# Performance work log

Measured on AMD Instinct MI355X. Metric: run time of the kernel, lower is better.

Reference implementation:

```python
import jax, jax.numpy as jnp
import numpy as np

EMBED_DIM = 1024
HEAD_DIM = 128

def setup_inputs() -> dict:
    key = jax.random.key(0)
    ks = jax.random.split(key, 7)
    B, S = 4, 2048
    x = jax.random.normal(ks[0], (B, S, EMBED_DIM), dtype=jnp.float32)
    # Linear params: weight [embed_dim, head_dim] (applied as x @ W + b), scaled init
    scale = 1.0 / np.sqrt(EMBED_DIM)
    Wq = jax.random.normal(ks[1], (EMBED_DIM, HEAD_DIM), dtype=jnp.float32) * scale
    Wk = jax.random.normal(ks[2], (EMBED_DIM, HEAD_DIM), dtype=jnp.float32) * scale
    Wv = jax.random.normal(ks[3], (EMBED_DIM, HEAD_DIM), dtype=jnp.float32) * scale
    bq = jax.random.normal(ks[4], (HEAD_DIM,), dtype=jnp.float32) * 0.01
    bk = jax.random.normal(ks[5], (HEAD_DIM,), dtype=jnp.float32) * 0.01
    bv = jax.random.normal(ks[6], (HEAD_DIM,), dtype=jnp.float32) * 0.01
    return {"x": x, "Wq": Wq, "bq": bq, "Wk": Wk, "bk": bk, "Wv": Wv, "bv": bv}

def reference(x, Wq, bq, Wk, bk, Wv, bv):
    # x: [B, S, E]
    S = x.shape[1]
    norm = jnp.asarray(HEAD_DIM ** 0.5, x.dtype)
    q = x @ Wq + bq  # [B, S, D]
    k = x @ Wk + bk
    v = x @ Wv + bv
    scores = jnp.einsum('bsd,btd->bst', q, k) / norm  # [B, S, S]
    causal = jnp.tril(jnp.ones((S, S), dtype=bool))
    scores = jnp.where(causal, scores, -jnp.inf)
    att = jax.nn.softmax(scores, axis=-1)
    return jnp.einsum('bst,btd->bsd', att, v)  # [B, S, D]
```

## Files before the change

### kernel.cpp

```cpp
#include <hip/hip_runtime.h>
#include <hip/hip_bf16.h>

typedef __attribute__((ext_vector_type(8))) short short8;
typedef __attribute__((ext_vector_type(4))) float f32x4;

static __device__ __forceinline__ unsigned short f2bf(float f){
  union { float f; unsigned int u; } v; v.f = f;
  unsigned int r = v.u + 0x7fffu + ((v.u >> 16) & 1u);
  return (unsigned short)(r >> 16);
}

static __device__ __forceinline__ void load_lds16(const unsigned short* g, unsigned short* l){
  __builtin_amdgcn_global_load_lds(
      (const __attribute__((address_space(1))) unsigned int*)(g),
      (__attribute__((address_space(3))) unsigned int*)(l), 16, 0, 0);
}

__global__ void k_prep(const float* __restrict__ Wq, const float* __restrict__ Wk,
                       const float* __restrict__ Wv,
                       const float* __restrict__ bq, const float* __restrict__ bk,
                       const float* __restrict__ bv,
                       unsigned short* __restrict__ Wt, float* __restrict__ bias){
  int gid = blockIdx.x * 256 + threadIdx.x;
  int p = gid >> 17;
  int rem = gid & 131071;
  int d = rem >> 10, e = rem & 1023;
  const float* W = (p==0) ? Wq : ((p==1) ? Wk : Wv);
  Wt[gid] = f2bf(W[e*128 + d]);
  if (gid < 384){
    int pp = gid >> 7, dd = gid & 127;
    bias[gid] = (pp==0) ? bq[dd] : ((pp==1) ? bk[dd] : bv[dd]);
  }
}

__global__ __launch_bounds__(256) void k_gemm_qkv(
    const float* __restrict__ x, const unsigned short* __restrict__ Wt,
    const float* __restrict__ bias,
    unsigned short* __restrict__ Qsw, unsigned short* __restrict__ Ksw,
    unsigned short* __restrict__ Vsw){
  __shared__ __align__(16) char smem[51200];
  float* Lf = (float*)smem;
  int tid = threadIdx.x;
  int bid = blockIdx.x;
  int xcd = bid & 7;
  int slot = bid >> 3;
  int mtl = slot / 3;
  int p   = slot - mtl*3;
  int mt  = xcd*16 + mtl;
  int m0 = mt * 64;
  int w = tid >> 6, lane = tid & 63, quad = lane >> 4, l16 = lane & 15;
  int wm = (w >> 1) * 32, wn = (w & 1) * 64;
  f32x4 acc[2][4];
  #pragma unroll
  for (int i=0;i<2;i++)
    #pragma unroll
    for (int j=0;j<4;j++) acc[i][j] = (f32x4){0.f,0.f,0.f,0.f};

  int arow = tid >> 2;
  int acg  = tid & 3;
  const float* Ax = x + (size_t)(m0 + arow)*1024 + acg*16;
  float4 av[4];

  const unsigned short* Wp = Wt + p * (128*1024);
  const unsigned short* Bg = Wp + (w*32 + (lane>>3))*1024 + (lane&7)*8;
  int boff = (w*32)*64;

  auto aload = [&](int k0){
    #pragma unroll
    for (int i=0;i<4;i++) av[i] = *(const float4*)(Ax + k0 + i*4);
  };
  auto astore = [&](int sel){
    unsigned short h[16];
    #pragma unroll
    for (int i=0;i<4;i++){
      h[i*4+0]=f2bf(av[i].x); h[i*4+1]=f2bf(av[i].y);
      h[i*4+2]=f2bf(av[i].z); h[i*4+3]=f2bf(av[i].w);
    }
    unsigned short* Ad = (unsigned short*)(smem + sel*25600) + arow*72 + acg*16;
    *(uint4*)(Ad)   = *(uint4*)(h);
    *(uint4*)(Ad+8) = *(uint4*)(h+8);
  };
  auto bstage = [&](int sel, int k0){
    unsigned short* Bl = (unsigned short*)(smem + sel*25600 + 9216) + boff;
    #pragma unroll
    for (int s8=0; s8<4; s8++) load_lds16(Bg + k0 + s8*8192, Bl + s8*512);
  };

  aload(0); bstage(0, 0); astore(0);
  __syncthreads();
  int cur = 0;
  for (int t=0; t<16; t++){
    if (t < 15){ aload((t+1)*64); bstage(cur^1, (t+1)*64); }
    const unsigned short* Ac = (const unsigned short*)(smem + cur*25600);
    const unsigned short* Bc = Ac + 4608;
    #pragma unroll
    for (int kk=0; kk<64; kk+=32){
      short8 af[2], bf[4];
      #pragma unroll
      for (int i=0;i<2;i++) af[i] = *(const short8*)(Ac + (wm + i*16 + l16)*72 + kk + quad*8);
      #pragma unroll
      for (int j=0;j<4;j++) bf[j] = *(const short8*)(Bc + (wn + j*16 + l16)*64 + kk + quad*8);
      #pragma unroll
      for (int i=0;i<2;i++)
        #pragma unroll
        for (int j=0;j<4;j++)
          acc[i][j] = __builtin_amdgcn_mfma_f32_16x16x32_bf16(af[i], bf[j], acc[i][j], 0,0,0);
    }
    if (t < 15) astore(cur^1);
    __syncthreads();
    cur ^= 1;
  }

  const float qscale = 0.08838834764831845f;
  if (p == 2){
    #pragma unroll
    for (int i=0;i<2;i++)
      #pragma unroll
      for (int j=0;j<4;j++){
        int grow0 = m0 + wm + i*16 + quad*4;
        int col = wn + j*16 + l16;
        unsigned short pk[4];
        float bv_ = bias[256 + col];
        #pragma unroll
        for (int r=0;r<4;r++) pk[r] = f2bf(acc[i][j][r] + bv_);
        int bb2 = grow0 >> 11, s = grow0 & 2047;
        int t64 = s >> 6, srem = s & 63;
        int kc2 = srem >> 5, q2 = (srem >> 3) & 3, jj = srem & 7;
        int nt = col >> 4, l2 = col & 15;
        *(uint2*)(Vsw + (bb2*32+t64)*8192 + nt*1024 + kc2*512 + q2*128 + l2*8 + jj) = *(uint2*)pk;
      }
  } else {
    #pragma unroll
    for (int i=0;i<2;i++)
      #pragma unroll
      for (int j=0;j<4;j++)
        #pragma unroll
        for (int r=0;r<4;r++)
          Lf[(wm + i*16 + quad*4 + r)*128 + wn + j*16 + l16] = acc[i][j][r];
    __syncthreads();
    unsigned short* dst = (p==0)? Qsw : Ksw;
    float scale = (p==0)? qscale : 1.0f;
    #pragma unroll
    for (int it=0; it<8; it++){
      int g = it*256 + tid;
      int row = g >> 5, cs = (g & 31)*4;
      f32x4 a = *(const f32x4*)(Lf + row*128 + cs);
      int grow = m0 + row;
      int rt = grow >> 4, m = grow & 15;
      int kc = cs >> 5, q2 = (cs >> 3) & 3, jj = cs & 7;
      unsigned short pk[4];
      #pragma unroll
      for (int k=0;k<4;k++) pk[k] = f2bf((a[k] + bias[p*128+cs+k])*scale);
      *(uint2*)(dst + rt*2048 + kc*512 + q2*128 + m*8 + jj) = *(uint2*)pk;
    }
  }
}

__global__ __launch_bounds__(256) void k_attn(
    const unsigned short* __restrict__ Qsw, const unsigned short* __restrict__ Ksw,
    const unsigned short* __restrict__ Vsw, float* __restrict__ out){
  __shared__ __align__(16) float Ob[4*2112];
  __shared__ float Ml[4][2][16];
  __shared__ __align__(16) unsigned short Pw[4*1280];
  int x = blockIdx.x;
  int b = x & 3;
  int qb = x >> 2;
  int T64 = (qb >> 2) + 1;
  int tid = threadIdx.x;
  int w = tid >> 6;
  int lane = tid & 63;
  int quad = lane >> 4, l16 = lane & 15;
  int qs = qb * 16;

  short8 aq[4];
  #pragma unroll
  for (int kc=0;kc<4;kc++)
    aq[kc] = *(const short8*)(Qsw + (b*128 + qb)*2048 + kc*512 + lane*8);

  f32x4 o[8];
  #pragma unroll
  for (int i=0;i<8;i++) o[i] = (f32x4){0.f,0.f,0.f,0.f};
  float mcol = -1e30f;
  float lcol = 0.f;
  short8 ap[2];
  unsigned short* Pws = Pw + w*1280;

  const unsigned short* Kb = Ksw + b*128*2048;
  const unsigned short* Vb = Vsw + b*32*8192;

  for (int tt = w; tt < T64; tt += 4){
    int t0 = tt * 64;
    short8 kf[16];
    #pragma unroll
    for (int nt=0;nt<4;nt++){
      const unsigned short* Kt = Kb + ((t0>>4)+nt)*2048 + lane*8;
      #pragma unroll
      for (int kc=0;kc<4;kc++)
        kf[nt*4+kc] = *(const short8*)(Kt + kc*512);
    }
    f32x4 sc[4];
    #pragma unroll
    for (int nt=0;nt<4;nt++) sc[nt] = (f32x4){0.f,0.f,0.f,0.f};
    __builtin_amdgcn_s_setprio(1);
    #pragma unroll
    for (int nt=0;nt<4;nt++)
      #pragma unroll
      for (int kc=0;kc<4;kc++)
        sc[nt] = __builtin_amdgcn_mfma_f32_16x16x32_bf16(kf[nt*4+kc], aq[kc], sc[nt], 0,0,0);
    __builtin_amdgcn_s_setprio(0);
    short8 vf[16];
    const unsigned short* Vt0 = Vb + (t0>>6)*8192 + lane*8;
    #pragma unroll
    for (int nt=0;nt<8;nt++)
      #pragma unroll
      for (int kc2=0;kc2<2;kc2++)
        vf[nt*2+kc2] = *(const short8*)(Vt0 + nt*1024 + kc2*512);

    if (t0 + 63 > qs){
      #pragma unroll
      for (int nt=0;nt<4;nt++){
        int kb_ = t0 + nt*16 + quad*4;
        #pragma unroll
        for (int r=0;r<4;r++)
          if (kb_ + r > qs + l16) sc[nt][r] = -1e30f;
      }
    }
    float mt_ = -1e30f;
    #pragma unroll
    for (int nt=0;nt<4;nt++)
      #pragma unroll
      for (int r=0;r<4;r++) mt_ = fmaxf(mt_, sc[nt][r]);
    mt_ = fmaxf(mt_, __shfl_xor(mt_, 16));
    mt_ = fmaxf(mt_, __shfl_xor(mt_, 32));
    float mn = fmaxf(mcol, mt_);
    float al = __expf(mcol - mn);
    mcol = mn;
    float ls = 0.f;
    #pragma unroll
    for (int nt=0;nt<4;nt++)
      #pragma unroll
      for (int r=0;r<4;r++){
        float pv = __expf(sc[nt][r] - mn);
        sc[nt][r] = pv;
        ls += pv;
      }
    ls += __shfl_xor(ls, 16);
    ls += __shfl_xor(ls, 32);
    lcol = lcol*al + ls;
    #pragma unroll
    for (int r=0;r<4;r++){
      float ar = __shfl(al, quad*4 + r);
      #pragma unroll
      for (int nt=0;nt<8;nt++) o[nt][r] *= ar;
    }
    #pragma unroll
    for (int nt=0;nt<4;nt++){
      unsigned short pk[4];
      #pragma unroll
      for (int r=0;r<4;r++) pk[r] = f2bf(sc[nt][r]);
      *(uint2*)(Pws + l16*80 + nt*16 + quad*4) = *(uint2*)pk;
    }
    ap[0] = *(const short8*)(Pws + l16*80 + quad*8);
    ap[1] = *(const short8*)(Pws + l16*80 + 32 + quad*8);
    __builtin_amdgcn_s_setprio(1);
    #pragma unroll
    for (int nt=0; nt<8; nt++)
      #pragma unroll
      for (int kc2=0;kc2<2;kc2++)
        o[nt] = __builtin_amdgcn_mfma_f32_16x16x32_bf16(ap[kc2], vf[nt*2+kc2], o[nt], 0,0,0);
    __builtin_amdgcn_s_setprio(0);
  }

  #pragma unroll
  for (int nt=0;nt<8;nt++)
    #pragma unroll
    for (int r=0;r<4;r++)
      Ob[w*2112 + (quad*4 + r)*132 + nt*16 + l16] = o[nt][r];
  if (quad == 0){
    Ml[w][0][l16] = mcol;
    Ml[w][1][l16] = lcol;
  }
  __syncthreads();

  int row = tid >> 4;
  int c0 = (tid & 15) * 8;
  float m0_ = fmaxf(fmaxf(Ml[0][0][row], Ml[1][0][row]),
                    fmaxf(Ml[2][0][row], Ml[3][0][row]));
  f32x4 acc0 = (f32x4){0.f,0.f,0.f,0.f};
  f32x4 acc1 = (f32x4){0.f,0.f,0.f,0.f};
  float lsum = 0.f;
  #pragma unroll
  for (int ww=0; ww<4; ww++){
    float e = __expf(Ml[ww][0][row] - m0_);
    lsum += Ml[ww][1][row] * e;
    const float* Or = Ob + ww*2112 + row*132 + c0;
    acc0 += *(const f32x4*)(Or)     * e;
    acc1 += *(const f32x4*)(Or + 4) * e;
  }
  float inv = 1.0f / lsum;
  float* op = out + (size_t)(b*2048 + qs + row)*128 + c0;
  acc0 *= inv; acc1 *= inv;
  *(f32x4*)(op)     = acc0;
  *(f32x4*)(op + 4) = acc1;
}

extern "C" void kernel_launch(void* const* d_in, const int* in_sizes, int n_in,
                              void* d_out, int out_size, void* d_ws, size_t ws_size,
                              hipStream_t stream) {
  const float* x  = (const float*)d_in[0];
  const float* Wq = (const float*)d_in[1];
  const float* bq = (const float*)d_in[2];
  const float* Wk = (const float*)d_in[3];
  const float* bk = (const float*)d_in[4];
  const float* Wv = (const float*)d_in[5];
  const float* bv = (const float*)d_in[6];
  char* ws = (char*)d_ws;
  unsigned short* Wt   = (unsigned short*)(ws);
  float*          bias = (float*)(ws + 786432);
  unsigned short* Qsw  = (unsigned short*)(ws + 788480);
  unsigned short* Ksw  = (unsigned short*)(ws + 2885632);
  unsigned short* Vsw  = (unsigned short*)(ws + 4982784);
  float* out = (float*)d_out;

  hipLaunchKernelGGL(k_prep,    dim3(1536),    dim3(256), 0, stream,
                     Wq, Wk, Wv, bq, bk, bv, Wt, bias);
  hipLaunchKernelGGL(k_gemm_qkv,dim3(384),     dim3(256), 0, stream,
                     x, Wt, bias, Qsw, Ksw, Vsw);
  hipLaunchKernelGGL(k_attn,    dim3(512),     dim3(256), 0, stream,
                     Qsw, Ksw, Vsw, out);
}
```

Before: 125.9 us.

## Fuse QKV projections per 32-row tile and reorder causal attention blocks

The QKV GEMM now has each 512-thread block compute all three projections (384 columns) for 32 rows of x. The previous version gave each block one of Q, K or V for 64 rows, so the same x rows were converted from fp32 to bf16 three times in separate blocks. The K step drops to 32 with XOR-swizzled LDS layouts for A and B to avoid bank conflicts. The attention kernel reorders query blocks so heavy and light causal tiles interleave for better load balance. The GEMM grid shrinks to 256 blocks, which may lower parallelism, and the smaller K step doubles the number of barrier iterations.

```diff
diff --git a/kernel.cpp b/kernel.cpp
--- a/kernel.cpp
+++ b/kernel.cpp
@@ -33,126 +33,120 @@
   }
 }
 
-__global__ __launch_bounds__(256) void k_gemm_qkv(
+__global__ __launch_bounds__(512) void k_gemm_qkv(
     const float* __restrict__ x, const unsigned short* __restrict__ Wt,
     const float* __restrict__ bias,
     unsigned short* __restrict__ Qsw, unsigned short* __restrict__ Ksw,
     unsigned short* __restrict__ Vsw){
-  __shared__ __align__(16) char smem[51200];
+  __shared__ __align__(16) char smem[53248];
   float* Lf = (float*)smem;
   int tid = threadIdx.x;
-  int bid = blockIdx.x;
-  int xcd = bid & 7;
-  int slot = bid >> 3;
-  int mtl = slot / 3;
-  int p   = slot - mtl*3;
-  int mt  = xcd*16 + mtl;
-  int m0 = mt * 64;
+  int m0 = blockIdx.x * 32;
   int w = tid >> 6, lane = tid & 63, quad = lane >> 4, l16 = lane & 15;
-  int wm = (w >> 1) * 32, wn = (w & 1) * 64;
-  f32x4 acc[2][4];
+  int wc0 = w * 48;
+  f32x4 acc[2][3];
   #pragma unroll
   for (int i=0;i<2;i++)
     #pragma unroll
-    for (int j=0;j<4;j++) acc[i][j] = (f32x4){0.f,0.f,0.f,0.f};
-
-  int arow = tid >> 2;
-  int acg  = tid & 3;
-  const float* Ax = x + (size_t)(m0 + arow)*1024 + acg*16;
-  float4 av[4];
-
-  const unsigned short* Wp = Wt + p * (128*1024);
-  const unsigned short* Bg = Wp + (w*32 + (lane>>3))*1024 + (lane&7)*8;
-  int boff = (w*32)*64;
-
-  auto aload = [&](int k0){
-    #pragma unroll
-    for (int i=0;i<4;i++) av[i] = *(const float4*)(Ax + k0 + i*4);
+    for (int j=0;j<3;j++) acc[i][j] = (f32x4){0.f,0.f,0.f,0.f};
+
+  int ar = tid >> 4, ac = tid & 15;
+  const float* Ax = x + (size_t)(m0 + ar)*1024 + ac*2;
+  float2 av;
+  unsigned int aoffB = ar*64 + (((ac>>2) ^ (ar&3))<<4) + (ac&3)*4;
+
+  const unsigned short* Bg = Wt + (size_t)(w*48 + (lane>>2))*1024
+                                + (((lane&3) ^ ((lane>>2)&3))*8);
+  int boffS = w*1536;
+
+  auto bstage = [&](int sel, int k0){
+    unsigned short* Bl = (unsigned short*)(smem + sel*26624 + 2048) + boffS;
+    #pragma unroll
+    for (int r=0;r<3;r++) load_lds16(Bg + k0 + r*16384, Bl + r*512);
   };
   auto astore = [&](int sel){
-    unsigned short h[16];
-    #pragma unroll
-    for (int i=0;i<4;i++){
-      h[i*4+0]=f2bf(av[i].x); h[i*4+1]=f2bf(av[i].y);
-      h[i*4+2]=f2bf(av[i].z); h[i*4+3]=f2bf(av[i].w);
-    }
-    unsigned short* Ad = (unsigned short*)(smem + sel*25600) + arow*72 + acg*16;
-    *(uint4*)(Ad)   = *(uint4*)(h);
-    *(uint4*)(Ad+8) = *(uint4*)(h+8);
+    unsigned short h[2];
+    h[0] = f2bf(av.x); h[1] = f2bf(av.y);
+    *(unsigned int*)(smem + sel*26624 + aoffB) = *(unsigned int*)h;
   };
-  auto bstage = [&](int sel, int k0){
-    unsigned short* Bl = (unsigned short*)(smem + sel*25600 + 9216) + boff;
-    #pragma unroll
-    for (int s8=0; s8<4; s8++) load_lds16(Bg + k0 + s8*8192, Bl + s8*512);
-  };
-
-  aload(0); bstage(0, 0); astore(0);
+
+  av = *(const float2*)(Ax);
+  bstage(0, 0);
+  astore(0);
   __syncthreads();
   int cur = 0;
-  for (int t=0; t<16; t++){
-    if (t < 15){ aload((t+1)*64); bstage(cur^1, (t+1)*64); }
-    const unsigned short* Ac = (const unsigned short*)(smem + cur*25600);
-    const unsigned short* Bc = Ac + 4608;
-    #pragma unroll
-    for (int kk=0; kk<64; kk+=32){
-      short8 af[2], bf[4];
-      #pragma unroll
-      for (int i=0;i<2;i++) af[i] = *(const short8*)(Ac + (wm + i*16 + l16)*72 + kk + quad*8);
-      #pragma unroll
-      for (int j=0;j<4;j++) bf[j] = *(const short8*)(Bc + (wn + j*16 + l16)*64 + kk + quad*8);
-      #pragma unroll
-      for (int i=0;i<2;i++)
-        #pragma unroll
-        for (int j=0;j<4;j++)
-          acc[i][j] = __builtin_amdgcn_mfma_f32_16x16x32_bf16(af[i], bf[j], acc[i][j], 0,0,0);
-    }
-    if (t < 15) astore(cur^1);
+  int swz = ((quad ^ (l16&3)) << 3);
+  for (int t=0; t<32; t++){
+    if (t < 31){ av = *(const float2*)(Ax + (t+1)*32); bstage(cur^1, (t+1)*32); }
+    const unsigned short* Ac = (const unsigned short*)(smem + cur*26624);
+    const unsigned short* Bc = Ac + 1024;
+    short8 af[2], bf[3];
+    #pragma unroll
+    for (int i=0;i<2;i++)
+      af[i] = *(const short8*)(Ac + (i*16 + l16)*32 + swz);
+    #pragma unroll
+    for (int j=0;j<3;j++)
+      bf[j] = *(const short8*)(Bc + (wc0 + j*16 + l16)*32 + swz);
+    #pragma unroll
+    for (int i=0;i<2;i++)
+      #pragma unroll
+      for (int j=0;j<3;j++)
+        acc[i][j] = __builtin_amdgcn_mfma_f32_16x16x32_bf16(af[i], bf[j], acc[i][j], 0,0,0);
+    if (t < 31) astore(cur^1);
     __syncthreads();
     cur ^= 1;
   }
 
+  #pragma unroll
+  for (int i=0;i<2;i++)
+    #pragma unroll
+    for (int j=0;j<3;j++)
+      #pragma unroll
+      for (int r=0;r<4;r++)
+        Lf[(i*16 + quad*4 + r)*384 + wc0 + j*16 + l16] = acc[i][j][r];
+  __syncthreads();
+
   const float qscale = 0.08838834764831845f;
-  if (p == 2){
-    #pragma unroll
-    for (int i=0;i<2;i++)
-      #pragma unroll
-      for (int j=0;j<4;j++){
-        int grow0 = m0 + wm + i*16 + quad*4;
-        int col = wn + j*16 + l16;
-        unsigned short pk[4];
-        float bv_ = bias[256 + col];
-        #pragma unroll
-        for (int r=0;r<4;r++) pk[r] = f2bf(acc[i][j][r] + bv_);
-        int bb2 = grow0 >> 11, s = grow0 & 2047;
-        int t64 = s >> 6, srem = s & 63;
-        int kc2 = srem >> 5, q2 = (srem >> 3) & 3, jj = srem & 7;
-        int nt = col >> 4, l2 = col & 15;
-        *(uint2*)(Vsw + (bb2*32+t64)*8192 + nt*1024 + kc2*512 + q2*128 + l2*8 + jj) = *(uint2*)pk;
-      }
-  } else {
-    #pragma unroll
-    for (int i=0;i<2;i++)
-      #pragma unroll
-      for (int j=0;j<4;j++)
-        #pragma unroll
-        for (int r=0;r<4;r++)
-          Lf[(wm + i*16 + quad*4 + r)*128 + wn + j*16 + l16] = acc[i][j][r];
-    __syncthreads();
-    unsigned short* dst = (p==0)? Qsw : Ksw;
-    float scale = (p==0)? qscale : 1.0f;
-    #pragma unroll
-    for (int it=0; it<8; it++){
-      int g = it*256 + tid;
-      int row = g >> 5, cs = (g & 31)*4;
-      f32x4 a = *(const f32x4*)(Lf + row*128 + cs);
-      int grow = m0 + row;
-      int rt = grow >> 4, m = grow & 15;
+  int row = tid >> 4;
+  int c0 = (tid & 15) * 8;
+  int grow = m0 + row;
+  int rt = grow >> 4, mm = grow & 15;
+  {
+    unsigned short pk[8];
+    #pragma unroll
+    for (int k=0;k<8;k++) pk[k] = f2bf((Lf[row*384 + c0 + k] + bias[c0 + k]) * qscale);
+    #pragma unroll
+    for (int h=0;h<2;h++){
+      int cs = c0 + h*4;
       int kc = cs >> 5, q2 = (cs >> 3) & 3, jj = cs & 7;
-      unsigned short pk[4];
-      #pragma unroll
-      for (int k=0;k<4;k++) pk[k] = f2bf((a[k] + bias[p*128+cs+k])*scale);
-      *(uint2*)(dst + rt*2048 + kc*512 + q2*128 + m*8 + jj) = *(uint2*)pk;
-    }
+      *(uint2*)(Qsw + rt*2048 + kc*512 + q2*128 + mm*8 + jj) = *(uint2*)(pk + h*4);
+    }
+  }
+  {
+    unsigned short pk[8];
+    #pragma unroll
+    for (int k=0;k<8;k++) pk[k] = f2bf(Lf[row*384 + 128 + c0 + k] + bias[128 + c0 + k]);
+    #pragma unroll
+    for (int h=0;h<2;h++){
+      int cs = c0 + h*4;
+      int kc = cs >> 5, q2 = (cs >> 3) & 3, jj = cs & 7;
+      *(uint2*)(Ksw + rt*2048 + kc*512 + q2*128 + mm*8 + jj) = *(uint2*)(pk + h*4);
+    }
+  }
+  #pragma unroll
+  for (int it=0; it<2; it++){
+    int g = it*512 + tid;
+    int col = g & 127, r0 = (g >> 7) * 4;
+    float bv_ = bias[256 + col];
+    unsigned short pk[4];
+    #pragma unroll
+    for (int k=0;k<4;k++) pk[k] = f2bf(Lf[(r0+k)*384 + 256 + col] + bv_);
+    int grow0 = m0 + r0;
+    int bb2 = grow0 >> 11, s = grow0 & 2047;
+    int t64 = s >> 6, srem = s & 63;
+    int kc2 = srem >> 5, q2 = (srem >> 3) & 3, jj = srem & 7;
+    int nt = col >> 4, l2 = col & 15;
+    *(uint2*)(Vsw + (size_t)(bb2*32+t64)*8192 + nt*1024 + kc2*512 + q2*128 + l2*8 + jj) = *(uint2*)pk;
   }
 }
 
@@ -164,7 +158,8 @@
   __shared__ __align__(16) unsigned short Pw[4*1280];
   int x = blockIdx.x;
   int b = x & 3;
-  int qb = x >> 2;
+  int q = x >> 2;
+  int qb = (q < 64) ? (q*2) : (255 - q*2);
   int T64 = (qb >> 2) + 1;
   int tid = threadIdx.x;
   int w = tid >> 6;
@@ -324,7 +319,7 @@
 
   hipLaunchKernelGGL(k_prep,    dim3(1536),    dim3(256), 0, stream,
                      Wq, Wk, Wv, bq, bk, bv, Wt, bias);
-  hipLaunchKernelGGL(k_gemm_qkv,dim3(384),     dim3(256), 0, stream,
+  hipLaunchKernelGGL(k_gemm_qkv,dim3(256),     dim3(512), 0, stream,
                      x, Wt, bias, Qsw, Ksw, Vsw);
   hipLaunchKernelGGL(k_attn,    dim3(512),     dim3(256), 0, stream,
                      Qsw, Ksw, Vsw, out);
```

Result: slower. 128.5 us (+2.0%).
